# Optimization experiments

Hardware: AMD Instinct MI355X
Metric: run time of the kernel (lower is better)

## Reference

```python
import jax, jax.numpy as jnp
import numpy as np
import math

N = 20000          # nodes
E = 320000         # edges (avg degree 16)
NS, NV = 16, 4     # scalar / vector multiplicities
NCAT = 10
CAT_VOCAB = 119
DIST_DIM = 32
LIG_MAX_R = 5.0
W1_NUMEL = NS * NS + NS * NV          # 320 : layer1 tp weights
W2_NUMEL = NS * NS + NV * NS + NS * NV + NV * NV + NV * NV  # 416


def setup_inputs() -> dict:
    key = jax.random.key(0)
    ks = jax.random.split(key, 24)
    s = 0.1
    inp = {
        'x_cat': jax.random.randint(ks[0], (N, NCAT), 0, 2),
        'x_scalar': jax.random.normal(ks[1], (N, 32), jnp.float32),
        'pos': jax.random.normal(ks[2], (N, 3), jnp.float32) * 3.0,
        'edge_index': jax.random.randint(ks[3], (2, E), 0, N),
        'edge_bond': jax.random.uniform(ks[4], (E, 10), jnp.float32),
        # AtomEncoder params
        'emb_tables': jax.random.normal(ks[5], (NCAT, CAT_VOCAB, NS)) * s,
        'node_w': jax.random.normal(ks[6], (32, NS)) * s,
        'node_b': jnp.zeros((NS,), jnp.float32),
        # lig_edge_embedding MLP (42 -> ns -> ns)
        'em_w1': jax.random.normal(ks[7], (10 + DIST_DIM, NS)) * s,
        'em_b1': jnp.zeros((NS,), jnp.float32),
        'em_w2': jax.random.normal(ks[8], (NS, NS)) * s,
        'em_b2': jnp.zeros((NS,), jnp.float32),
        'c1_w1': jax.random.normal(ks[9], (3 * NS, 3 * NS)) * s,
        'c1_b1': jnp.zeros((3 * NS,), jnp.float32),
        'c1_w2': jax.random.normal(ks[10], (3 * NS, W1_NUMEL)) * s,
        'c1_b2': jnp.zeros((W1_NUMEL,), jnp.float32),
        # conv layer 2 fc
        'c2_w1': jax.random.normal(ks[11], (3 * NS, 3 * NS)) * s,
        'c2_b1': jnp.zeros((3 * NS,), jnp.float32),
        'c2_w2': jax.random.normal(ks[12], (3 * NS, W2_NUMEL)) * s,
        'c2_b2': jnp.zeros((W2_NUMEL,), jnp.float32),
    }
    return inp


def _scatter_mean(vals, idx, n):
    s = jax.ops.segment_sum(vals, idx, num_segments=n)
    cnt = jax.ops.segment_sum(jnp.ones(idx.shape, vals.dtype), idx, num_segments=n)
    return s / jnp.maximum(cnt, 1.0)[:, None]


def _forward(x_cat, x_scalar, pos, edge_index, edge_bond,
             emb_tables, node_w, node_b, em_w1, em_b1, em_w2, em_b2,
             c1_w1, c1_b1, c1_w2, c1_b2, c2_w1, c2_b1, c2_w2, c2_b2):
    ns, nv = NS, NV
    n = x_cat.shape[0]
    # ---- AtomEncoder: sum of categorical embeddings + linear(scalar) ----
    gathered = emb_tables[jnp.arange(NCAT)[None, :], x_cat]      # [N, 10, ns]
    node = gathered.sum(axis=1) + x_scalar @ node_w + node_b    # [N, ns]

    src, dst = edge_index[0], edge_index[1]
    vec = pos[dst] - pos[src]                                   # [E, 3]
    dist = jnp.sqrt(jnp.sum(vec * vec, axis=-1) + 1e-12)
    unit = vec / (dist + 1e-8)[:, None]
    # spherical harmonics, lmax=1, component normalization: [1, sqrt(3)*r_hat]
    sh0 = jnp.ones((vec.shape[0], 1), vec.dtype)
    sh1 = math.sqrt(3.0) * unit                                 # [E, 3]

    # ---- GaussianSmearing + edge embedding MLP ----
    offset = jnp.linspace(0.0, LIG_MAX_R, DIST_DIM)
    coeff = -0.5 / float(LIG_MAX_R / (DIST_DIM - 1)) ** 2
    demb = jnp.exp(coeff * (dist[:, None] - offset[None, :]) ** 2)
    e_in = jnp.concatenate([edge_bond, demb], axis=1)           # [E, 42]
    edge_emb = jax.nn.relu(e_in @ em_w1 + em_b1) @ em_w2 + em_b2  # [E, ns]

    # ======== conv layer 1: ns x0e -> ns x0e + nv x1o ========
    ea = jnp.concatenate([edge_emb, node[src, :ns], node[dst, :ns]], axis=1)
    w = jax.nn.relu(ea @ c1_w1 + c1_b1) @ c1_w2 + c1_b2         # [E, 320]
    wa = w[:, :ns * ns].reshape(-1, ns, ns)
    wb = w[:, ns * ns:].reshape(-1, ns, nv)
    s_dst = node[dst]                                           # [E, ns]
    a = 1.0 / math.sqrt(ns)                                     # fan-in norm
    out0 = jnp.einsum('euk,eu->ek', wa, s_dst) * sh0 * a        # 0e x 0e -> 0e
    out1 = jnp.einsum('euw,eu->ew', wb, s_dst)[:, :, None] * sh1[:, None, :] * a
    tp = jnp.concatenate([out0, out1.reshape(-1, 3 * nv)], axis=1)
    node = _scatter_mean(tp, src, n)                            # [N, ns+3nv]

    # ======== conv layer 2: ns x0e + nv x1o -> ns x0e + nv x1o + nv x1e ====
    ea = jnp.concatenate([edge_emb, node[src, :ns], node[dst, :ns]], axis=1)
    w = jax.nn.relu(ea @ c2_w1 + c2_b1) @ c2_w2 + c2_b2         # [E, 416]
    o = 0
    wa = w[:, o:o + ns * ns].reshape(-1, ns, ns); o += ns * ns
    wb = w[:, o:o + nv * ns].reshape(-1, nv, ns); o += nv * ns
    wc = w[:, o:o + ns * nv].reshape(-1, ns, nv); o += ns * nv
    wd = w[:, o:o + nv * nv].reshape(-1, nv, nv); o += nv * nv
    we = w[:, o:o + nv * nv].reshape(-1, nv, nv)
    s = node[dst, :ns]
    v = node[dst, ns:].reshape(-1, nv, 3)
    a0 = 1.0 / math.sqrt(ns + nv)   # two paths into 0e
    a1 = 1.0 / math.sqrt(ns + nv)   # two paths into 1o
    aE = 1.0 / math.sqrt(nv)        # one path into 1e
    vdot = jnp.einsum('evi,ei->ev', v, sh1)                     # 1o . 1o
    out0 = (jnp.einsum('euk,eu->ek', wa, s) * sh0
            + jnp.einsum('euk,eu->ek', wb, vdot) / math.sqrt(3.0)) * a0
    out1o = (jnp.einsum('euw,eu->ew', wc, s)[:, :, None] * sh1[:, None, :]
             + jnp.einsum('euw,eui->ewi', wd, v) * sh0[:, :, None]) * a1
    crossv = jnp.cross(v, jnp.broadcast_to(sh1[:, None, :], v.shape))
    out1e = jnp.einsum('euw,eui->ewi', we, crossv) * (aE / math.sqrt(2.0))
    tp = jnp.concatenate([out0, out1o.reshape(-1, 3 * nv),
                          out1e.reshape(-1, 3 * nv)], axis=1)
    node = _scatter_mean(tp, src, n)                            # [N, ns+6nv] = [N,40]
    return node


def reference(x_cat, x_scalar, pos, edge_index, edge_bond,
              emb_tables, node_w, node_b, em_w1, em_b1, em_w2, em_b2,
              c1_w1, c1_b1, c1_w2, c1_b2, c2_w1, c2_b1, c2_w2, c2_b2):
    return _forward(x_cat, x_scalar, pos, edge_index, edge_bond,
                    emb_tables, node_w, node_b, em_w1, em_b1, em_w2, em_b2,
                    c1_w1, c1_b1, c1_w2, c1_b2, c2_w1, c2_b1, c2_w2, c2_b2)
```

## Files before the change

kernel.cpp:

```cpp
#include <hip/hip_runtime.h>
#include <math.h>

#define NN 20000
#define NE 320000

typedef _Float16 f16x8 __attribute__((ext_vector_type(8)));
typedef float f32x4 __attribute__((ext_vector_type(4)));
typedef unsigned short ushort_t;
typedef unsigned int uint_t;

#define MFMA16(A,B,C) __builtin_amdgcn_mfma_f32_16x16x32_f16((A),(B),(C),0,0,0)
#define LDS_FENCE() do{ asm volatile("s_waitcnt lgkmcnt(0)" ::: "memory"); __builtin_amdgcn_sched_barrier(0);}while(0)

static_assert(NE % 256 == 0, "edge grid must tile exactly");

__device__ __forceinline__ float frelu(float x){ return fmaxf(x, 0.0f); }

__device__ __forceinline__ void splitf(float x, ushort_t& h, ushort_t& l){
    _Float16 hh = (_Float16)x;
    float r = (x - (float)hh) * 2048.0f;
    _Float16 ll = (_Float16)r;
    union { _Float16 f; ushort_t u; } ch, cl;
    ch.f = hh; cl.f = ll;
    h = ch.u; l = cl.u;
}

__device__ __forceinline__ void edge_embed(
    int e, int s, int d,
    const float* __restrict__ pos,
    const float* __restrict__ edge_bond,
    const float* __restrict__ em_w1, const float* __restrict__ em_b1,
    const float* __restrict__ em_w2, const float* __restrict__ em_b2,
    float* eemb, float* sh1)
{
    float vx = pos[d*3+0] - pos[s*3+0];
    float vy = pos[d*3+1] - pos[s*3+1];
    float vz = pos[d*3+2] - pos[s*3+2];
    float d2 = vx*vx + vy*vy + vz*vz + 1e-12f;
    float dist = sqrtf(d2);
    float inv = 1.0f / (dist + 1e-8f);
    const float SQ3 = 1.7320508075688772f;
    sh1[0] = SQ3 * vx * inv;
    sh1[1] = SQ3 * vy * inv;
    sh1[2] = SQ3 * vz * inv;

    float ein[42];
    #pragma unroll
    for (int t = 0; t < 10; ++t) ein[t] = edge_bond[e*10 + t];
    const float coeff = -19.22f;
    const float step  = 5.0f / 31.0f;
    #pragma unroll
    for (int k = 0; k < 32; ++k) {
        float dd = dist - step * (float)k;
        ein[10+k] = __expf(coeff * dd * dd);
    }

    float t1[16];
    #pragma unroll
    for (int j = 0; j < 16; ++j) t1[j] = em_b1[j];
    #pragma unroll
    for (int t = 0; t < 42; ++t) {
        float v = ein[t];
        #pragma unroll
        for (int j = 0; j < 16; ++j) t1[j] += v * em_w1[t*16 + j];
    }
    #pragma unroll
    for (int j = 0; j < 16; ++j) t1[j] = frelu(t1[j]);

    #pragma unroll
    for (int j = 0; j < 16; ++j) eemb[j] = em_b2[j];
    #pragma unroll
    for (int t = 0; t < 16; ++t) {
        float v = t1[t];
        #pragma unroll
        for (int j = 0; j < 16; ++j) eemb[j] += v * em_w2[t*16 + j];
    }
}

__global__ __launch_bounds__(256)
void k_edge_pre(const int* __restrict__ ei, const float* __restrict__ pos,
                const float* __restrict__ edge_bond,
                const float* __restrict__ em_w1, const float* __restrict__ em_b1,
                const float* __restrict__ em_w2, const float* __restrict__ em_b2,
                float* __restrict__ eembG, float* __restrict__ eshG,
                float* __restrict__ cnt)
{
    int e = blockIdx.x*256 + threadIdx.x;
    int s = ei[e], d = ei[NE + e];
    float em[16], sh1[3];
    edge_embed(e, s, d, pos, edge_bond, em_w1, em_b1, em_w2, em_b2, em, sh1);
    float4* pe = reinterpret_cast<float4*>(eembG + (size_t)e*16);
    #pragma unroll
    for (int k = 0; k < 4; ++k)
        pe[k] = make_float4(em[4*k], em[4*k+1], em[4*k+2], em[4*k+3]);
    reinterpret_cast<float4*>(eshG)[e] = make_float4(sh1[0], sh1[1], sh1[2], 0.f);
    atomicAdd(cnt + s, 1.0f);
}

__global__ __launch_bounds__(256)
void k_node_y(const float* __restrict__ node, int stride,
              const float* __restrict__ w1, float* __restrict__ y)
{
    int n = blockIdx.x*256 + threadIdx.x;
    if (n >= NN) return;
    float sv[16];
    const float4* r = reinterpret_cast<const float4*>(node + (size_t)n*stride);
    #pragma unroll
    for (int k = 0; k < 4; ++k) {
        float4 q = r[k];
        sv[4*k]=q.x; sv[4*k+1]=q.y; sv[4*k+2]=q.z; sv[4*k+3]=q.w;
    }
    float yb[48];
    #pragma unroll
    for (int j = 0; j < 48; ++j) yb[j] = 0.f;
    #pragma unroll
    for (int t = 0; t < 16; ++t) {
        float v = sv[t];
        #pragma unroll
        for (int j = 0; j < 48; ++j) yb[j] += v * w1[(16+t)*48 + j];
    }
    float* yo = y + (size_t)n*96;
    #pragma unroll
    for (int j = 0; j < 12; ++j)
        reinterpret_cast<float4*>(yo)[j] = make_float4(yb[4*j], yb[4*j+1], yb[4*j+2], yb[4*j+3]);
    #pragma unroll
    for (int j = 0; j < 48; ++j) yb[j] = 0.f;
    #pragma unroll
    for (int t = 0; t < 16; ++t) {
        float v = sv[t];
        #pragma unroll
        for (int j = 0; j < 48; ++j) yb[j] += v * w1[(32+t)*48 + j];
    }
    #pragma unroll
    for (int j = 0; j < 12; ++j)
        reinterpret_cast<float4*>(yo + 48)[j] = make_float4(yb[4*j], yb[4*j+1], yb[4*j+2], yb[4*j+3]);
}

__global__ __launch_bounds__(256)
void k_pack(const float* __restrict__ w2, const float* __restrict__ b2,
            ushort_t* __restrict__ out, int NC, int ntiles)
{
    int slot = blockIdx.x*256 + threadIdx.x;
    if (slot >= ntiles*128) return;
    int tl = slot >> 7; int r7 = slot & 127; int kb = r7 >> 6; int ll = r7 & 63;
    int col = tl*16 + (ll & 15);
    int k0 = (kb<<5) + ((ll>>4)<<3);
    uint_t hw[4], lw[4];
    #pragma unroll
    for (int p = 0; p < 4; ++p) {
        int ka = k0 + 2*p, kb2 = k0 + 2*p + 1;
        float va = (ka < 48) ? w2[ka*NC + col] : (ka == 48 ? b2[col] : 0.0f);
        float vb = (kb2 < 48) ? w2[kb2*NC + col] : (kb2 == 48 ? b2[col] : 0.0f);
        ushort_t ah, al, bh, bl;
        splitf(va, ah, al);
        splitf(vb, bh, bl);
        hw[p] = (uint_t)ah | ((uint_t)bh << 16);
        lw[p] = (uint_t)al | ((uint_t)bl << 16);
    }
    int base = tl*2048 + kb*1024 + ll*8;
    *reinterpret_cast<uint4*>(&out[base])       = make_uint4(hw[0], hw[1], hw[2], hw[3]);
    *reinterpret_cast<uint4*>(&out[base + 512]) = make_uint4(lw[0], lw[1], lw[2], lw[3]);
}

struct B4 { f16x8 h0, l0, h1, l1; };
__device__ __forceinline__ B4 loadB(const f16x8* __restrict__ g, int t, int l) {
    B4 b;
    const f16x8* p = g + t*256 + l;
    b.h0 = p[0];
    b.l0 = p[64];
    b.h1 = p[128];
    b.l1 = p[192];
    return b;
}

__device__ __forceinline__ void stage_A(ushort_t* bounce, int l,
                                        const uint_t* hph, const uint_t* hpl,
                                        f16x8 ahi[4][2], f16x8 alo[4][2])
{
    #pragma unroll
    for (int t = 0; t < 4; ++t)
        *reinterpret_cast<uint4*>(&bounce[l*32 + t*8]) = make_uint4(0,0,0,0);
    LDS_FENCE();
    #pragma unroll
    for (int mt = 0; mt < 4; ++mt) {
        if ((l >> 4) == mt) {
            #pragma unroll
            for (int jj = 0; jj < 25; ++jj) {
                int k = jj*2, kb = k >> 5, kk = k & 31;
                int lr = (l & 15) + ((kk >> 3) << 4);
                int off = kb*512 + lr*8 + (kk & 7);
                *reinterpret_cast<uint_t*>(&bounce[off])        = hph[jj];
                *reinterpret_cast<uint_t*>(&bounce[1024 + off]) = hpl[jj];
            }
        }
        LDS_FENCE();
        ahi[mt][0] = *reinterpret_cast<const f16x8*>(&bounce[l*8]);
        ahi[mt][1] = *reinterpret_cast<const f16x8*>(&bounce[512 + l*8]);
        alo[mt][0] = *reinterpret_cast<const f16x8*>(&bounce[1024 + l*8]);
        alo[mt][1] = *reinterpret_cast<const f16x8*>(&bounce[1536 + l*8]);
        LDS_FENCE();
    }
}

__device__ __forceinline__ void build_h(
    int e, int s, int d,
    const float* __restrict__ eembG,
    const float* __restrict__ y,
    const float* __restrict__ w1, const float* __restrict__ b1,
    float* h)
{
    float em[16];
    const float4* pe = reinterpret_cast<const float4*>(eembG + (size_t)e*16);
    #pragma unroll
    for (int k = 0; k < 4; ++k) {
        float4 q = pe[k];
        em[4*k]=q.x; em[4*k+1]=q.y; em[4*k+2]=q.z; em[4*k+3]=q.w;
    }
    #pragma unroll
    for (int j = 0; j < 48; ++j) h[j] = b1[j];
    #pragma unroll
    for (int t = 0; t < 16; ++t) {
        float v = em[t];
        #pragma unroll
        for (int j = 0; j < 48; ++j) h[j] += v * w1[t*48 + j];
    }
    const float4* pb = reinterpret_cast<const float4*>(y + (size_t)s*96);
    const float4* pc = reinterpret_cast<const float4*>(y + (size_t)d*96 + 48);
    #pragma unroll
    for (int kk = 0; kk < 12; ++kk) {
        float4 qb = pb[kk], qc = pc[kk];
        h[4*kk+0] = frelu(h[4*kk+0] + qb.x + qc.x);
        h[4*kk+1] = frelu(h[4*kk+1] + qb.y + qc.y);
        h[4*kk+2] = frelu(h[4*kk+2] + qb.z + qc.z);
        h[4*kk+3] = frelu(h[4*kk+3] + qb.w + qc.w);
    }
}

__global__ __launch_bounds__(256)
void k_node_feat(const int* __restrict__ x_cat, const float* __restrict__ x_scalar,
                 const float* __restrict__ emb, const float* __restrict__ node_w,
                 const float* __restrict__ node_b, float* __restrict__ node0)
{
    int n = blockIdx.x * 256 + threadIdx.x;
    if (n >= NN) return;
    float acc[16];
    #pragma unroll
    for (int k = 0; k < 16; ++k) acc[k] = node_b[k];
    #pragma unroll
    for (int c = 0; c < 10; ++c) {
        int idx = x_cat[n*10 + c];
        const float4* row = reinterpret_cast<const float4*>(emb + (c*119 + idx)*16);
        #pragma unroll
        for (int k = 0; k < 4; ++k) {
            float4 q = row[k];
            acc[4*k+0] += q.x; acc[4*k+1] += q.y; acc[4*k+2] += q.z; acc[4*k+3] += q.w;
        }
    }
    #pragma unroll
    for (int t = 0; t < 32; ++t) {
        float xs = x_scalar[n*32 + t];
        #pragma unroll
        for (int k = 0; k < 16; ++k) acc[k] += xs * node_w[t*16 + k];
    }
    #pragma unroll
    for (int k = 0; k < 16; ++k) node0[n*16 + k] = acc[k];
}

__global__ __launch_bounds__(256)
void k_edge_l1(const int* __restrict__ ei,
               const float* __restrict__ w1, const float* __restrict__ b1,
               const ushort_t* __restrict__ packW,
               const float* __restrict__ eembG, const float* __restrict__ eshG,
               const float* __restrict__ y,
               const float* __restrict__ node0,
               float* __restrict__ accum)
{
    __shared__ __align__(16) unsigned char smem[20736];
    float* sT  = (float*)smem;
    float* sSh = (float*)(smem + 16640);
    int*   sSrc= (int*)(smem + 19712);

    int tid = threadIdx.x;
    int l = tid & 63;
    int cc = l & 15;
    int e = blockIdx.x*256 + tid;
    int s = ei[e], d = ei[NE + e];

    float4 shv = reinterpret_cast<const float4*>(eshG)[e];
    float sd[16];
    {
        const float4* rd = reinterpret_cast<const float4*>(node0 + (size_t)d*16);
        #pragma unroll
        for (int k = 0; k < 4; ++k) {
            float4 q = rd[k];
            sd[4*k]=q.x; sd[4*k+1]=q.y; sd[4*k+2]=q.z; sd[4*k+3]=q.w;
        }
    }
    float h[48];
    build_h(e, s, d, eembG, y, w1, b1, h);

    uint_t hph[25], hpl[25];
    #pragma unroll
    for (int jj = 0; jj < 24; ++jj) {
        ushort_t ah, al, bh, bl;
        splitf(h[2*jj],   ah, al);
        splitf(h[2*jj+1], bh, bl);
        hph[jj] = (uint_t)ah | ((uint_t)bh << 16);
        hpl[jj] = (uint_t)al | ((uint_t)bl << 16);
    }
    hph[24] = 0x3C00u;
    hpl[24] = 0u;

    f16x8 ahi[4][2], alo[4][2];
    stage_A((ushort_t*)smem + (tid >> 6)*2048, l, hph, hpl, ahi, alo);

    __syncthreads();
    sSrc[tid] = s;
    #pragma unroll
    for (int u = 0; u < 16; ++u) sT[u*260 + tid] = sd[u];
    sSh[tid*3+0] = shv.x; sSh[tid*3+1] = shv.y; sSh[tid*3+2] = shv.z;
    __syncthreads();

    f32x4 out0[4];
    float ob[4][4];
    #pragma unroll
    for (int mt = 0; mt < 4; ++mt) {
        out0[mt] = (f32x4){0.f,0.f,0.f,0.f};
        #pragma unroll
        for (int r = 0; r < 4; ++r) ob[mt][r] = 0.f;
    }

    const f16x8* gB = reinterpret_cast<const f16x8*>(packW);

    auto process = [&](int t, const B4& cur) {
        #pragma unroll
        for (int mt = 0; mt < 4; ++mt) {
            f32x4 Dh = (f32x4){0.f,0.f,0.f,0.f};
            f32x4 Dc = (f32x4){0.f,0.f,0.f,0.f};
            Dh = MFMA16(ahi[mt][0], cur.h0, Dh);
            Dh = MFMA16(ahi[mt][1], cur.h1, Dh);
            Dc = MFMA16(alo[mt][0], cur.h0, Dc);
            Dc = MFMA16(ahi[mt][0], cur.l0, Dc);
            Dc = MFMA16(alo[mt][1], cur.h1, Dc);
            Dc = MFMA16(ahi[mt][1], cur.l1, Dc);
            f32x4 D = Dh + Dc * 0.00048828125f;
            int elb = (tid & 192) + (mt << 4) + ((l >> 4) << 2);
            if (t < 16) {
                f32x4 sv = *reinterpret_cast<const f32x4*>(&sT[t*260 + elb]);
                out0[mt] += sv * D;
            } else {
                const float* sp = &sT[(((t-16)<<2) + (cc>>2))*260 + elb];
                #pragma unroll
                for (int r = 0; r < 4; ++r) ob[mt][r] += sp[r] * D[r];
            }
        }
    };

    B4 b0 = loadB(gB, 0, l), b1v = loadB(gB, 1, l);
    #pragma unroll 1
    for (int t = 0; t < 20; t += 2) {
        B4 p0 = (t + 2 < 20) ? loadB(gB, t + 2, l) : b0;
        process(t, b0);
        B4 p1 = (t + 3 < 20) ? loadB(gB, t + 3, l) : b1v;
        process(t + 1, b1v);
        b0 = p0; b1v = p1;
    }

    #pragma unroll
    for (int mt = 0; mt < 4; ++mt) {
        int elb = (tid & 192) + (mt << 4) + ((l >> 4) << 2);
        #pragma unroll
        for (int r = 0; r < 4; ++r) {
            int el = elb + r;
            int sidx = sSrc[el];
            atomicAdd(accum + (size_t)sidx*28 + cc, out0[mt][r] * 0.25f);
            float x = ob[mt][r];
            x += __shfl_xor(x, 4); x += __shfl_xor(x, 8);
            int q = cc / 3; int i = cc - q*3;
            float xq = __shfl(x, (l & 48) | q);
            if (cc < 12)
                atomicAdd(accum + (size_t)sidx*28 + 16 + cc, 0.25f * xq * sSh[el*3 + i]);
        }
    }
}

__global__ __launch_bounds__(256)
void k_edge_l2(const int* __restrict__ ei,
               const float* __restrict__ w1, const float* __restrict__ b1,
               const ushort_t* __restrict__ packW,
               const float* __restrict__ eembG, const float* __restrict__ eshG,
               const float* __restrict__ y,
               const float* __restrict__ node1,
               float* __restrict__ accum2)
{
    __shared__ __align__(16) unsigned char smem[37376];
    float* sT  = (float*)smem;
    float* sVd = (float*)(smem + 16640);
    float* sV  = (float*)(smem + 20800);
    float* sSh = (float*)(smem + 33280);
    int*   sSrc= (int*)(smem + 36352);

    int tid = threadIdx.x;
    int l = tid & 63;
    int cc = l & 15;
    int e = blockIdx.x*256 + tid;
    int s = ei[e], d = ei[NE + e];

    float4 shv = reinterpret_cast<const float4*>(eshG)[e];
    float sh1[3] = {shv.x, shv.y, shv.z};
    float sd[16], vv[12];
    {
        const float4* rd = reinterpret_cast<const float4*>(node1 + (size_t)d*28);
        #pragma unroll
        for (int k = 0; k < 4; ++k) {
            float4 q = rd[k];
            sd[4*k]=q.x; sd[4*k+1]=q.y; sd[4*k+2]=q.z; sd[4*k+3]=q.w;
        }
        #pragma unroll
        for (int k = 0; k < 3; ++k) {
            float4 q = rd[4+k];
            vv[4*k]=q.x; vv[4*k+1]=q.y; vv[4*k+2]=q.z; vv[4*k+3]=q.w;
        }
    }
    float vdr[4];
    const float INV_SQ3 = 0.5773502691896258f;
    #pragma unroll
    for (int u = 0; u < 4; ++u)
        vdr[u] = (vv[u*3]*sh1[0] + vv[u*3+1]*sh1[1] + vv[u*3+2]*sh1[2]) * INV_SQ3;

    float h[48];
    build_h(e, s, d, eembG, y, w1, b1, h);

    uint_t hph[25], hpl[25];
    #pragma unroll
    for (int jj = 0; jj < 24; ++jj) {
        ushort_t ah, al, bh, bl;
        splitf(h[2*jj],   ah, al);
        splitf(h[2*jj+1], bh, bl);
        hph[jj] = (uint_t)ah | ((uint_t)bh << 16);
        hpl[jj] = (uint_t)al | ((uint_t)bl << 16);
    }
    hph[24] = 0x3C00u;
    hpl[24] = 0u;

    f16x8 ahi[4][2], alo[4][2];
    stage_A((ushort_t*)smem + (tid >> 6)*2048, l, hph, hpl, ahi, alo);

    __syncthreads();
    sSrc[tid] = s;
    #pragma unroll
    for (int u = 0; u < 16; ++u) sT[u*260 + tid] = sd[u];
    #pragma unroll
    for (int u = 0; u < 4; ++u) sVd[u*260 + tid] = vdr[u];
    #pragma unroll
    for (int k = 0; k < 12; ++k) sV[k*260 + tid] = vv[k];
    sSh[tid*3+0] = shv.x; sSh[tid*3+1] = shv.y; sSh[tid*3+2] = shv.z;
    __syncthreads();

    const float A0 = 0.22360679774997896f;
    const float AE = 0.3535533905932738f;

    f32x4 out0[4];
    float outc[4][4];
    #pragma unroll
    for (int mt = 0; mt < 4; ++mt) {
        out0[mt] = (f32x4){0.f,0.f,0.f,0.f};
        #pragma unroll
        for (int r = 0; r < 4; ++r) outc[mt][r] = 0.f;
    }

    const f16x8* gB = reinterpret_cast<const f16x8*>(packW);

    auto process = [&](int t, const B4& cur) {
        #pragma unroll
        for (int mt = 0; mt < 4; ++mt) {
            f32x4 Dh = (f32x4){0.f,0.f,0.f,0.f};
            f32x4 Dc = (f32x4){0.f,0.f,0.f,0.f};
            Dh = MFMA16(ahi[mt][0], cur.h0, Dh);
            Dh = MFMA16(ahi[mt][1], cur.h1, Dh);
            Dc = MFMA16(alo[mt][0], cur.h0, Dc);
            Dc = MFMA16(ahi[mt][0], cur.l0, Dc);
            Dc = MFMA16(alo[mt][1], cur.h1, Dc);
            Dc = MFMA16(ahi[mt][1], cur.l1, Dc);
            f32x4 D = Dh + Dc * 0.00048828125f;
            int elb = (tid & 192) + (mt << 4) + ((l >> 4) << 2);
            if (t < 16) {
                f32x4 sv = *reinterpret_cast<const f32x4*>(&sT[t*260 + elb]);
                out0[mt] += sv * D;
            } else if (t < 20) {
                f32x4 vd = *reinterpret_cast<const f32x4*>(&sVd[(t-16)*260 + elb]);
                out0[mt] += vd * D;
            } else if (t < 24) {
                const float* sp = &sT[(((t-20)<<2) + (cc>>2))*260 + elb];
                #pragma unroll
                for (int r = 0; r < 4; ++r) outc[mt][r] += sp[r] * D[r];
            } else if (t == 24) {
                int base3 = (cc >> 2) * 3;
                #pragma unroll
                for (int r = 0; r < 4; ++r) {
                    int el = elb + r;
                    float vx = sV[(base3+0)*260 + el];
                    float vy = sV[(base3+1)*260 + el];
                    float vz = sV[(base3+2)*260 + el];
                    float a0 = D[r]*vx, a1 = D[r]*vy, a2 = D[r]*vz;
                    a0 += __shfl_xor(a0,4); a0 += __shfl_xor(a0,8);
                    a1 += __shfl_xor(a1,4); a1 += __shfl_xor(a1,8);
                    a2 += __shfl_xor(a2,4); a2 += __shfl_xor(a2,8);
                    float xc = outc[mt][r];
                    xc += __shfl_xor(xc,4); xc += __shfl_xor(xc,8);
                    int q = cc / 3; int i = cc - q*3;
                    int srcl = (l & 48) | q;
                    float g0 = __shfl(a0, srcl), g1 = __shfl(a1, srcl), g2 = __shfl(a2, srcl);
                    float oo = (i==0) ? g0 : ((i==1) ? g1 : g2);
                    float xq = __shfl(xc, srcl);
                    if (cc < 12) {
                        float sh1i = sSh[el*3 + i];
                        atomicAdd(accum2 + (size_t)sSrc[el]*40 + 16 + cc,
                                  A0 * (xq * sh1i + oo));
                    }
                }
            } else {
                int base3 = (cc >> 2) * 3;
                #pragma unroll
                for (int r = 0; r < 4; ++r) {
                    int el = elb + r;
                    float vx = sV[(base3+0)*260 + el];
                    float vy = sV[(base3+1)*260 + el];
                    float vz = sV[(base3+2)*260 + el];
                    float sx = sSh[el*3+0], sy = sSh[el*3+1], sz = sSh[el*3+2];
                    float cx = vy*sz - vz*sy;
                    float cy = vz*sx - vx*sz;
                    float cz = vx*sy - vy*sx;
                    float a0 = D[r]*cx, a1 = D[r]*cy, a2 = D[r]*cz;
                    a0 += __shfl_xor(a0,4); a0 += __shfl_xor(a0,8);
                    a1 += __shfl_xor(a1,4); a1 += __shfl_xor(a1,8);
                    a2 += __shfl_xor(a2,4); a2 += __shfl_xor(a2,8);
                    int q = cc / 3; int i = cc - q*3;
                    int srcl = (l & 48) | q;
                    float g0 = __shfl(a0, srcl), g1 = __shfl(a1, srcl), g2 = __shfl(a2, srcl);
                    float oo = (i==0) ? g0 : ((i==1) ? g1 : g2);
                    if (cc < 12)
                        atomicAdd(accum2 + (size_t)sSrc[el]*40 + 28 + cc, AE * oo);
                }
            }
        }
    };

    B4 b0 = loadB(gB, 0, l), b1v = loadB(gB, 1, l);
    #pragma unroll 1
    for (int t = 0; t < 26; t += 2) {
        B4 p0 = (t + 2 < 26) ? loadB(gB, t + 2, l) : b0;
        process(t, b0);
        B4 p1 = (t + 3 < 26) ? loadB(gB, t + 3, l) : b1v;
        process(t + 1, b1v);
        b0 = p0; b1v = p1;
    }

    #pragma unroll
    for (int mt = 0; mt < 4; ++mt) {
        int elb = (tid & 192) + (mt << 4) + ((l >> 4) << 2);
        #pragma unroll
        for (int r = 0; r < 4; ++r) {
            int el = elb + r;
            atomicAdd(accum2 + (size_t)sSrc[el]*40 + cc, out0[mt][r] * A0);
        }
    }
}

__global__ __launch_bounds__(256)
void k_div(const float* in, float* out, const float* __restrict__ cnt, int cols, int total)
{
    int i = blockIdx.x * 256 + threadIdx.x;
    if (i >= total) return;
    int n = i / cols;
    out[i] = in[i] / fmaxf(cnt[n], 1.0f);
}

extern "C" void kernel_launch(void* const* d_in, const int* in_sizes, int n_in,
                              void* d_out, int out_size, void* d_ws, size_t ws_size,
                              hipStream_t stream) {
    const int*   x_cat     = (const int*)  d_in[0];
    const float* x_scalar  = (const float*)d_in[1];
    const float* pos       = (const float*)d_in[2];
    const int*   ei        = (const int*)  d_in[3];
    const float* edge_bond = (const float*)d_in[4];
    const float* emb       = (const float*)d_in[5];
    const float* node_w    = (const float*)d_in[6];
    const float* node_b    = (const float*)d_in[7];
    const float* em_w1     = (const float*)d_in[8];
    const float* em_b1     = (const float*)d_in[9];
    const float* em_w2     = (const float*)d_in[10];
    const float* em_b2     = (const float*)d_in[11];
    const float* c1_w1     = (const float*)d_in[12];
    const float* c1_b1     = (const float*)d_in[13];
    const float* c1_w2     = (const float*)d_in[14];
    const float* c1_b2     = (const float*)d_in[15];
    const float* c2_w1     = (const float*)d_in[16];
    const float* c2_b1     = (const float*)d_in[17];
    const float* c2_w2     = (const float*)d_in[18];
    const float* c2_b2     = (const float*)d_in[19];

    float* ws     = (float*)d_ws;
    float* node0  = ws;
    float* accum1 = ws + 320000;
    float* accum2 = ws + 880000;
    float* cnt    = ws + 1680000;
    ushort_t* packA = (ushort_t*)(ws + 1700000);
    ushort_t* packB = packA + 20*2048;
    float* eembG  = ws + 1747104;
    float* eshG   = ws + 6867104;
    float* yBuf   = ws + 8147104;

    hipMemsetAsync(accum1, 0, (size_t)(560000 + 800000 + 20000) * sizeof(float), stream);

    k_pack<<<(20*128 + 255) / 256, 256, 0, stream>>>(c1_w2, c1_b2, packA, 320, 20);
    k_pack<<<(26*128 + 255) / 256, 256, 0, stream>>>(c2_w2, c2_b2, packB, 416, 26);

    k_node_feat<<<(NN + 255) / 256, 256, 0, stream>>>(
        x_cat, x_scalar, emb, node_w, node_b, node0);

    k_edge_pre<<<NE / 256, 256, 0, stream>>>(
        ei, pos, edge_bond, em_w1, em_b1, em_w2, em_b2, eembG, eshG, cnt);

    k_node_y<<<(NN + 255) / 256, 256, 0, stream>>>(node0, 16, c1_w1, yBuf);

    k_edge_l1<<<NE / 256, 256, 0, stream>>>(
        ei, c1_w1, c1_b1, packA, eembG, eshG, yBuf, node0, accum1);

    k_div<<<(560000 + 255) / 256, 256, 0, stream>>>(accum1, accum1, cnt, 28, 560000);

    k_node_y<<<(NN + 255) / 256, 256, 0, stream>>>(accum1, 28, c2_w1, yBuf);

    k_edge_l2<<<NE / 256, 256, 0, stream>>>(
        ei, c2_w1, c2_b1, packB, eembG, eshG, yBuf, accum1, accum2);

    k_div<<<(800000 + 255) / 256, 256, 0, stream>>>(accum2, (float*)d_out, cnt, 40, 800000);
}
```

Before: 345.1 us.

## Fuse edge preprocessing into layer-1 edge kernel and replicate scatter accumulators

The separate edge-preprocessing kernel is merged into the layer-1 edge kernel, so the edge embedding and spherical harmonics are computed in registers and used directly instead of being read back from global memory. They are still stored for layer 2. The scatter-add targets are also split into four copies chosen by block index, which spreads atomic contention; a new reduction-division kernel sums the copies. In exchange the accumulator memsets and the final reduction touch four times more memory, and the fused kernel may use more registers.

```diff
diff --git a/kernel.cpp b/kernel.cpp
--- a/kernel.cpp
+++ b/kernel.cpp
@@ -3,6 +3,7 @@
 
 #define NN 20000
 #define NE 320000
+#define NCPY 4
 
 typedef _Float16 f16x8 __attribute__((ext_vector_type(8)));
 typedef float f32x4 __attribute__((ext_vector_type(4)));
@@ -78,26 +79,6 @@
 }
 
 __global__ __launch_bounds__(256)
-void k_edge_pre(const int* __restrict__ ei, const float* __restrict__ pos,
-                const float* __restrict__ edge_bond,
-                const float* __restrict__ em_w1, const float* __restrict__ em_b1,
-                const float* __restrict__ em_w2, const float* __restrict__ em_b2,
-                float* __restrict__ eembG, float* __restrict__ eshG,
-                float* __restrict__ cnt)
-{
-    int e = blockIdx.x*256 + threadIdx.x;
-    int s = ei[e], d = ei[NE + e];
-    float em[16], sh1[3];
-    edge_embed(e, s, d, pos, edge_bond, em_w1, em_b1, em_w2, em_b2, em, sh1);
-    float4* pe = reinterpret_cast<float4*>(eembG + (size_t)e*16);
-    #pragma unroll
-    for (int k = 0; k < 4; ++k)
-        pe[k] = make_float4(em[4*k], em[4*k+1], em[4*k+2], em[4*k+3]);
-    reinterpret_cast<float4*>(eshG)[e] = make_float4(sh1[0], sh1[1], sh1[2], 0.f);
-    atomicAdd(cnt + s, 1.0f);
-}
-
-__global__ __launch_bounds__(256)
 void k_node_y(const float* __restrict__ node, int stride,
               const float* __restrict__ w1, float* __restrict__ y)
 {
@@ -202,20 +183,12 @@
     }
 }
 
-__device__ __forceinline__ void build_h(
-    int e, int s, int d,
-    const float* __restrict__ eembG,
+__device__ __forceinline__ void build_h_reg(
+    const float* em, int s, int d,
     const float* __restrict__ y,
     const float* __restrict__ w1, const float* __restrict__ b1,
     float* h)
 {
-    float em[16];
-    const float4* pe = reinterpret_cast<const float4*>(eembG + (size_t)e*16);
-    #pragma unroll
-    for (int k = 0; k < 4; ++k) {
-        float4 q = pe[k];
-        em[4*k]=q.x; em[4*k+1]=q.y; em[4*k+2]=q.z; em[4*k+3]=q.w;
-    }
     #pragma unroll
     for (int j = 0; j < 48; ++j) h[j] = b1[j];
     #pragma unroll
@@ -267,13 +240,16 @@
 }
 
 __global__ __launch_bounds__(256)
-void k_edge_l1(const int* __restrict__ ei,
+void k_edge_l1(const int* __restrict__ ei, const float* __restrict__ pos,
+               const float* __restrict__ edge_bond,
+               const float* __restrict__ em_w1, const float* __restrict__ em_b1,
+               const float* __restrict__ em_w2, const float* __restrict__ em_b2,
                const float* __restrict__ w1, const float* __restrict__ b1,
                const ushort_t* __restrict__ packW,
-               const float* __restrict__ eembG, const float* __restrict__ eshG,
                const float* __restrict__ y,
                const float* __restrict__ node0,
-               float* __restrict__ accum)
+               float* __restrict__ eembG, float* __restrict__ eshG,
+               float* __restrict__ accumC, float* __restrict__ cnt)
 {
     __shared__ __align__(16) unsigned char smem[20736];
     float* sT  = (float*)smem;
@@ -285,8 +261,19 @@
     int cc = l & 15;
     int e = blockIdx.x*256 + tid;
     int s = ei[e], d = ei[NE + e];
-
-    float4 shv = reinterpret_cast<const float4*>(eshG)[e];
+    float* __restrict__ accum = accumC + (size_t)(blockIdx.x & (NCPY-1)) * (NN*28);
+
+    float em[16], sh1[3];
+    edge_embed(e, s, d, pos, edge_bond, em_w1, em_b1, em_w2, em_b2, em, sh1);
+    {
+        float4* pe = reinterpret_cast<float4*>(eembG + (size_t)e*16);
+        #pragma unroll
+        for (int k = 0; k < 4; ++k)
+            pe[k] = make_float4(em[4*k], em[4*k+1], em[4*k+2], em[4*k+3]);
+        reinterpret_cast<float4*>(eshG)[e] = make_float4(sh1[0], sh1[1], sh1[2], 0.f);
+    }
+    atomicAdd(cnt + s, 1.0f);
+
     float sd[16];
     {
         const float4* rd = reinterpret_cast<const float4*>(node0 + (size_t)d*16);
@@ -297,7 +284,7 @@
         }
     }
     float h[48];
-    build_h(e, s, d, eembG, y, w1, b1, h);
+    build_h_reg(em, s, d, y, w1, b1, h);
 
     uint_t hph[25], hpl[25];
     #pragma unroll
@@ -318,7 +305,7 @@
     sSrc[tid] = s;
     #pragma unroll
     for (int u = 0; u < 16; ++u) sT[u*260 + tid] = sd[u];
-    sSh[tid*3+0] = shv.x; sSh[tid*3+1] = shv.y; sSh[tid*3+2] = shv.z;
+    sSh[tid*3+0] = sh1[0]; sSh[tid*3+1] = sh1[1]; sSh[tid*3+2] = sh1[2];
     __syncthreads();
 
     f32x4 out0[4];
@@ -391,7 +378,7 @@
                const float* __restrict__ eembG, const float* __restrict__ eshG,
                const float* __restrict__ y,
                const float* __restrict__ node1,
-               float* __restrict__ accum2)
+               float* __restrict__ accumC)
 {
     __shared__ __align__(16) unsigned char smem[37376];
     float* sT  = (float*)smem;
@@ -405,6 +392,7 @@
     int cc = l & 15;
     int e = blockIdx.x*256 + tid;
     int s = ei[e], d = ei[NE + e];
+    float* __restrict__ accum2 = accumC + (size_t)(blockIdx.x & (NCPY-1)) * (NN*40);
 
     float4 shv = reinterpret_cast<const float4*>(eshG)[e];
     float sh1[3] = {shv.x, shv.y, shv.z};
@@ -428,8 +416,17 @@
     for (int u = 0; u < 4; ++u)
         vdr[u] = (vv[u*3]*sh1[0] + vv[u*3+1]*sh1[1] + vv[u*3+2]*sh1[2]) * INV_SQ3;
 
+    float em[16];
+    {
+        const float4* pe = reinterpret_cast<const float4*>(eembG + (size_t)e*16);
+        #pragma unroll
+        for (int k = 0; k < 4; ++k) {
+            float4 q = pe[k];
+            em[4*k]=q.x; em[4*k+1]=q.y; em[4*k+2]=q.z; em[4*k+3]=q.w;
+        }
+    }
     float h[48];
-    build_h(e, s, d, eembG, y, w1, b1, h);
+    build_h_reg(em, s, d, y, w1, b1, h);
 
     uint_t hph[25], hpl[25];
     #pragma unroll
@@ -454,7 +451,7 @@
     for (int u = 0; u < 4; ++u) sVd[u*260 + tid] = vdr[u];
     #pragma unroll
     for (int k = 0; k < 12; ++k) sV[k*260 + tid] = vv[k];
-    sSh[tid*3+0] = shv.x; sSh[tid*3+1] = shv.y; sSh[tid*3+2] = shv.z;
+    sSh[tid*3+0] = sh1[0]; sSh[tid*3+1] = sh1[1]; sSh[tid*3+2] = sh1[2];
     __syncthreads();
 
     const float A0 = 0.22360679774997896f;
@@ -568,12 +565,16 @@
 }
 
 __global__ __launch_bounds__(256)
-void k_div(const float* in, float* out, const float* __restrict__ cnt, int cols, int total)
+void k_divm(const float* __restrict__ in, int stride, float* __restrict__ out,
+            const float* __restrict__ cnt, int cols, int total)
 {
     int i = blockIdx.x * 256 + threadIdx.x;
     if (i >= total) return;
     int n = i / cols;
-    out[i] = in[i] / fmaxf(cnt[n], 1.0f);
+    float sum = 0.f;
+    #pragma unroll
+    for (int c = 0; c < NCPY; ++c) sum += in[(size_t)c*stride + i];
+    out[i] = sum / fmaxf(cnt[n], 1.0f);
 }
 
 extern "C" void kernel_launch(void* const* d_in, const int* in_sizes, int n_in,
@@ -600,18 +601,19 @@
     const float* c2_w2     = (const float*)d_in[18];
     const float* c2_b2     = (const float*)d_in[19];
 
-    float* ws     = (float*)d_ws;
-    float* node0  = ws;
-    float* accum1 = ws + 320000;
-    float* accum2 = ws + 880000;
-    float* cnt    = ws + 1680000;
-    ushort_t* packA = (ushort_t*)(ws + 1700000);
+    float* ws    = (float*)d_ws;
+    float* node0 = ws;
+    float* cnt   = ws + 320000;
+    ushort_t* packA = (ushort_t*)(ws + 340000);
     ushort_t* packB = packA + 20*2048;
-    float* eembG  = ws + 1747104;
-    float* eshG   = ws + 6867104;
-    float* yBuf   = ws + 8147104;
-
-    hipMemsetAsync(accum1, 0, (size_t)(560000 + 800000 + 20000) * sizeof(float), stream);
+    float* eembG = ws + 400000;
+    float* eshG  = ws + 5520000;
+    float* yBuf  = ws + 6800000;
+    float* node1 = ws + 8720000;
+    float* accumC= ws + 9280000;
+
+    hipMemsetAsync(cnt, 0, 20000 * sizeof(float), stream);
+    hipMemsetAsync(accumC, 0, (size_t)NCPY * NN * 28 * sizeof(float), stream);
 
     k_pack<<<(20*128 + 255) / 256, 256, 0, stream>>>(c1_w2, c1_b2, packA, 320, 20);
     k_pack<<<(26*128 + 255) / 256, 256, 0, stream>>>(c2_w2, c2_b2, packB, 416, 26);
@@ -619,20 +621,20 @@
     k_node_feat<<<(NN + 255) / 256, 256, 0, stream>>>(
         x_cat, x_scalar, emb, node_w, node_b, node0);
 
-    k_edge_pre<<<NE / 256, 256, 0, stream>>>(
-        ei, pos, edge_bond, em_w1, em_b1, em_w2, em_b2, eembG, eshG, cnt);
-
     k_node_y<<<(NN + 255) / 256, 256, 0, stream>>>(node0, 16, c1_w1, yBuf);
 
     k_edge_l1<<<NE / 256, 256, 0, stream>>>(
-        ei, c1_w1, c1_b1, packA, eembG, eshG, yBuf, node0, accum1);
-
-    k_div<<<(560000 + 255) / 256, 256, 0, stream>>>(accum1, accum1, cnt, 28, 560000);
-
-    k_node_y<<<(NN + 255) / 256, 256, 0, stream>>>(accum1, 28, c2_w1, yBuf);
+        ei, pos, edge_bond, em_w1, em_b1, em_w2, em_b2,
+        c1_w1, c1_b1, packA, yBuf, node0, eembG, eshG, accumC, cnt);
+
+    k_divm<<<(560000 + 255) / 256, 256, 0, stream>>>(accumC, NN*28, node1, cnt, 28, 560000);
+
+    hipMemsetAsync(accumC, 0, (size_t)NCPY * NN * 40 * sizeof(float), stream);
+
+    k_node_y<<<(NN + 255) / 256, 256, 0, stream>>>(node1, 28, c2_w1, yBuf);
 
     k_edge_l2<<<NE / 256, 256, 0, stream>>>(
-        ei, c2_w1, c2_b1, packB, eembG, eshG, yBuf, accum1, accum2);
-
-    k_div<<<(800000 + 255) / 256, 256, 0, stream>>>(accum2, (float*)d_out, cnt, 40, 800000);
-}
+        ei, c2_w1, c2_b1, packB, eembG, eshG, yBuf, node1, accumC);
+
+    k_divm<<<(800000 + 255) / 256, 256, 0, stream>>>(accumC, NN*40, (float*)d_out, cnt, 40, 800000);
+}
```

After: 333.2 us. 3.4% less time.
